# Kernel optimization log

Hardware: AMD Instinct MI355X
Metric: run time of the kernel (lower is better)

The kernel has to match this reference:

```python
import jax, jax.numpy as jnp
import numpy as np

RADIUS = 2  # matches LGA(radius=2)


def setup_inputs() -> dict:
    key = jax.random.key(0)
    k1, k2 = jax.random.split(key)
    N, C, H, W = 4, 32, 384, 768
    K = 2 * RADIUS + 1
    input1 = jax.random.normal(k1, (N, C, H, W), dtype=jnp.float32)
    input2 = jax.random.uniform(k2, (N, K * K, H, W), dtype=jnp.float32)
    return {"input1": input1, "input2": input2}


def reference(input1, input2):
    # Local Guided Aggregation (GANet LGA):
    # out[n,c,h,w] = sum_{i,j in (2r+1)^2} input1[n,c,h+i-r,w+j-r] * input2[n,i*K+j,h,w]
    # Per-pixel 5x5 filter shared across channels; zero padding at borders.
    r = RADIUS
    K = 2 * r + 1
    N, C, H, W = input1.shape
    padded = jnp.pad(input1, ((0, 0), (0, 0), (r, r), (r, r)))
    out = jnp.zeros_like(input1)
    for i in range(K):
        for j in range(K):
            # shifted window [N,C,H,W] times per-pixel tap weight [N,1,H,W]
            out = out + padded[:, :, i:i + H, j:j + W] * input2[:, i * K + j][:, None, :, :]
    return out
```

## Files before the change

### kernel.cpp

```cpp
#include <hip/hip_runtime.h>


#define N_DIM 4
#define C_DIM 32
#define H_DIM 384
#define W_DIM 768
#define HW (H_DIM * W_DIM)
#define TH 4
#define TW 256
#define LROWS (TH + 4)
#define LW 260
#define CHUNKS (LROWS * 65)

__global__ __launch_bounds__(256, 3)
void lga_kernel(const float* __restrict__ in1,
                const float* __restrict__ in2,
                float* __restrict__ out) {
    __shared__ float lds[2][LROWS * LW];

    const int tid = threadIdx.x;
    const int tx  = tid & 63;
    const int ty  = tid >> 6;
    const int w0  = blockIdx.x * TW;
    const int h0  = blockIdx.y * TH;
    const int n   = blockIdx.z;

    const int h  = h0 + ty;
    const int wb = w0 + 4 * tx;

    float4 wt[25];
    {
        const float* w_src = in2 + ((size_t)n * 25) * HW + (size_t)h * W_DIM + wb;
#pragma unroll
        for (int t = 0; t < 25; ++t) {
            float4 v = *(const float4*)(w_src + (size_t)t * HW);
            asm volatile("" : "+v"(v.x), "+v"(v.y), "+v"(v.z), "+v"(v.w));
            wt[t] = v;
        }
    }

    const float* in1_n = in1 + (size_t)n * C_DIM * HW;
    float*       out_n = out + (size_t)n * C_DIM * HW;

    int  soff[3];
    int  ldst[3];
    int  gcol[3];
    bool fast[3];
    bool rok[3];
    bool act[3];
#pragma unroll
    for (int k = 0; k < 3; ++k) {
        const int idx = tid + 256 * k;
        act[k] = (k < 2) || (tid < CHUNKS - 512);
        const int row = idx / 65;
        const int c4  = idx - row * 65;
        const int gh  = h0 - 2 + row;
        const int g   = w0 - 2 + 4 * c4;
        rok[k]  = (unsigned)gh < H_DIM;
        gcol[k] = g;
        fast[k] = rok[k] && (g >= 0) && (g + 3 < W_DIM);
        soff[k] = (rok[k] ? gh : 0) * W_DIM + g;
        ldst[k] = row * LW + 4 * c4;
    }

    auto load_chunk = [&](const float* src, int k) -> float4 {
        float4 v;
        if (fast[k]) {
            const float* p = src + soff[k];
            const float2 a = *(const float2*)p;
            const float2 b = *(const float2*)(p + 2);
            v = make_float4(a.x, a.y, b.x, b.y);
        } else {
            const int g = gcol[k];
            const float* prow = src + (soff[k] - g);
            v.x = (rok[k] && (unsigned)(g + 0) < W_DIM) ? prow[g + 0] : 0.f;
            v.y = (rok[k] && (unsigned)(g + 1) < W_DIM) ? prow[g + 1] : 0.f;
            v.z = (rok[k] && (unsigned)(g + 2) < W_DIM) ? prow[g + 2] : 0.f;
            v.w = (rok[k] && (unsigned)(g + 3) < W_DIM) ? prow[g + 3] : 0.f;
        }
        return v;
    };

    {
        float4 v0 = load_chunk(in1_n, 0);
        float4 v1 = load_chunk(in1_n, 1);
        float4 v2 = make_float4(0.f, 0.f, 0.f, 0.f);
        if (act[2]) v2 = load_chunk(in1_n, 2);
        *(float4*)&lds[0][ldst[0]] = v0;
        *(float4*)&lds[0][ldst[1]] = v1;
        if (act[2]) *(float4*)&lds[0][ldst[2]] = v2;
    }
    __syncthreads();

    for (int c = 0; c < C_DIM; ++c) {
        const int  cur  = c & 1;
        const bool more = (c + 1 < C_DIM);

        float4 n0, n1, n2 = make_float4(0.f, 0.f, 0.f, 0.f);
        if (more) {
            const float* src = in1_n + (size_t)(c + 1) * HW;
            n0 = load_chunk(src, 0);
            n1 = load_chunk(src, 1);
            if (act[2]) n2 = load_chunk(src, 2);
        }

        float acc0 = 0.f, acc1 = 0.f, acc2 = 0.f, acc3 = 0.f;
        const float* lbase = &lds[cur][0];
#pragma unroll
        for (int i = 0; i < 5; ++i) {
            const float* lrow = lbase + (ty + i) * LW + 4 * tx;
            const float4 A = *(const float4*)lrow;
            const float4 B = *(const float4*)(lrow + 4);
            const float win[8] = {A.x, A.y, A.z, A.w, B.x, B.y, B.z, B.w};
#pragma unroll
            for (int j = 0; j < 5; ++j) {
                const float4 wv = wt[5 * i + j];
                acc0 += wv.x * win[j + 0];
                acc1 += wv.y * win[j + 1];
                acc2 += wv.z * win[j + 2];
                acc3 += wv.w * win[j + 3];
            }
        }

        *(float4*)(out_n + (size_t)c * HW + (size_t)h * W_DIM + wb)
            = make_float4(acc0, acc1, acc2, acc3);

        if (more) {
            float* dst = &lds[cur ^ 1][0];
            *(float4*)&dst[ldst[0]] = n0;
            *(float4*)&dst[ldst[1]] = n1;
            if (act[2]) *(float4*)&dst[ldst[2]] = n2;
            __syncthreads();
        }
    }
}

extern "C" void kernel_launch(void* const* d_in, const int* in_sizes, int n_in,
                              void* d_out, int out_size, void* d_ws, size_t ws_size,
                              hipStream_t stream) {
    const float* in1 = (const float*)d_in[0];
    const float* in2 = (const float*)d_in[1];
    float* out = (float*)d_out;
    dim3 grid(W_DIM / TW, H_DIM / TH, N_DIM);
    lga_kernel<<<grid, 256, 0, stream>>>(in1, in2, out);
}
```

Baseline: 418.8 us.

## Split channels across blocks, reload weights per channel, remap block order

Splits the 32-channel loop across 4 workgroups per spatial tile, so the grid is 4x larger. The 25 per-pixel float4 weights are no longer held in registers; they are re-read from global memory (likely L1/L2 hits) inside every channel iteration, and the launch bound is raised to 6 blocks per SM. A 1D grid with a swizzled block index groups the channel-split blocks of one tile together for cache locality. The cost is four times more weight traffic and halo reloads against higher occupancy and parallelism.

```diff
diff --git a/kernel.cpp b/kernel.cpp
--- a/kernel.cpp
+++ b/kernel.cpp
@@ -8,39 +8,38 @@
 #define HW (H_DIM * W_DIM)
 #define TH 4
 #define TW 256
+#define CSPLIT 4
+#define CPB (C_DIM / CSPLIT)
 #define LROWS (TH + 4)
 #define LW 260
 #define CHUNKS (LROWS * 65)
+#define NTILE ((W_DIM / TW) * (H_DIM / TH) * N_DIM)
+#define NWG (NTILE * CSPLIT)
 
-__global__ __launch_bounds__(256, 3)
+__global__ __launch_bounds__(256, 6)
 void lga_kernel(const float* __restrict__ in1,
                 const float* __restrict__ in2,
                 float* __restrict__ out) {
     __shared__ float lds[2][LROWS * LW];
 
+    const int b = blockIdx.x;
+    const int T = (b & 7) * (NWG / 8) + (b >> 3);
+    const int cs = T & 3;
+    const int t  = T >> 2;
+    const int bx = t % 3;
+    const int by = (t / 3) % (H_DIM / TH);
+    const int n  = t / (3 * (H_DIM / TH));
+    const int c0 = cs * CPB;
+
     const int tid = threadIdx.x;
     const int tx  = tid & 63;
     const int ty  = tid >> 6;
-    const int w0  = blockIdx.x * TW;
-    const int h0  = blockIdx.y * TH;
-    const int n   = blockIdx.z;
+    const int w0  = bx * TW;
+    const int h0  = by * TH;
+    const int h   = h0 + ty;
+    const int wb  = w0 + 4 * tx;
 
-    const int h  = h0 + ty;
-    const int wb = w0 + 4 * tx;
-
-    float4 wt[25];
-    {
-        const float* w_src = in2 + ((size_t)n * 25) * HW + (size_t)h * W_DIM + wb;
-#pragma unroll
-        for (int t = 0; t < 25; ++t) {
-            float4 v = *(const float4*)(w_src + (size_t)t * HW);
-            asm volatile("" : "+v"(v.x), "+v"(v.y), "+v"(v.z), "+v"(v.w));
-            wt[t] = v;
-        }
-    }
-
-    const float* in1_n = in1 + (size_t)n * C_DIM * HW;
-    float*       out_n = out + (size_t)n * C_DIM * HW;
+    const float* w_src = in2 + ((size_t)n * 25) * HW + (size_t)h * W_DIM + wb;
 
     int  soff[3];
     int  ldst[3];
@@ -68,8 +67,8 @@
         if (fast[k]) {
             const float* p = src + soff[k];
             const float2 a = *(const float2*)p;
-            const float2 b = *(const float2*)(p + 2);
-            v = make_float4(a.x, a.y, b.x, b.y);
+            const float2 b2 = *(const float2*)(p + 2);
+            v = make_float4(a.x, a.y, b2.x, b2.y);
         } else {
             const int g = gcol[k];
             const float* prow = src + (soff[k] - g);
@@ -81,27 +80,31 @@
         return v;
     };
 
+    const float* src0 = in1 + (size_t)n * C_DIM * HW + (size_t)c0 * HW;
+    float*       dst  = out + (size_t)n * C_DIM * HW + (size_t)c0 * HW
+                            + (size_t)h * W_DIM + wb;
+
     {
-        float4 v0 = load_chunk(in1_n, 0);
-        float4 v1 = load_chunk(in1_n, 1);
+        float4 v0 = load_chunk(src0, 0);
+        float4 v1 = load_chunk(src0, 1);
         float4 v2 = make_float4(0.f, 0.f, 0.f, 0.f);
-        if (act[2]) v2 = load_chunk(in1_n, 2);
+        if (act[2]) v2 = load_chunk(src0, 2);
         *(float4*)&lds[0][ldst[0]] = v0;
         *(float4*)&lds[0][ldst[1]] = v1;
         if (act[2]) *(float4*)&lds[0][ldst[2]] = v2;
     }
     __syncthreads();
 
-    for (int c = 0; c < C_DIM; ++c) {
-        const int  cur  = c & 1;
-        const bool more = (c + 1 < C_DIM);
+    for (int cc = 0; cc < CPB; ++cc) {
+        const int  cur  = cc & 1;
+        const bool more = (cc + 1 < CPB);
 
         float4 n0, n1, n2 = make_float4(0.f, 0.f, 0.f, 0.f);
         if (more) {
-            const float* src = in1_n + (size_t)(c + 1) * HW;
-            n0 = load_chunk(src, 0);
-            n1 = load_chunk(src, 1);
-            if (act[2]) n2 = load_chunk(src, 2);
+            const float* srcn = src0 + (size_t)(cc + 1) * HW;
+            n0 = load_chunk(srcn, 0);
+            n1 = load_chunk(srcn, 1);
+            if (act[2]) n2 = load_chunk(srcn, 2);
         }
 
         float acc0 = 0.f, acc1 = 0.f, acc2 = 0.f, acc3 = 0.f;
@@ -112,24 +115,26 @@
             const float4 A = *(const float4*)lrow;
             const float4 B = *(const float4*)(lrow + 4);
             const float win[8] = {A.x, A.y, A.z, A.w, B.x, B.y, B.z, B.w};
+            float4 wv[5];
+#pragma unroll
+            for (int j = 0; j < 5; ++j)
+                wv[j] = *(const float4*)(w_src + (size_t)(5 * i + j) * HW);
 #pragma unroll
             for (int j = 0; j < 5; ++j) {
-                const float4 wv = wt[5 * i + j];
-                acc0 += wv.x * win[j + 0];
-                acc1 += wv.y * win[j + 1];
-                acc2 += wv.z * win[j + 2];
-                acc3 += wv.w * win[j + 3];
+                acc0 += wv[j].x * win[j + 0];
+                acc1 += wv[j].y * win[j + 1];
+                acc2 += wv[j].z * win[j + 2];
+                acc3 += wv[j].w * win[j + 3];
             }
         }
 
-        *(float4*)(out_n + (size_t)c * HW + (size_t)h * W_DIM + wb)
-            = make_float4(acc0, acc1, acc2, acc3);
+        *(float4*)(dst + (size_t)cc * HW) = make_float4(acc0, acc1, acc2, acc3);
 
         if (more) {
-            float* dst = &lds[cur ^ 1][0];
-            *(float4*)&dst[ldst[0]] = n0;
-            *(float4*)&dst[ldst[1]] = n1;
-            if (act[2]) *(float4*)&dst[ldst[2]] = n2;
+            float* dbuf = &lds[cur ^ 1][0];
+            *(float4*)&dbuf[ldst[0]] = n0;
+            *(float4*)&dbuf[ldst[1]] = n1;
+            if (act[2]) *(float4*)&dbuf[ldst[2]] = n2;
             __syncthreads();
         }
     }
@@ -141,6 +146,5 @@
     const float* in1 = (const float*)d_in[0];
     const float* in2 = (const float*)d_in[1];
     float* out = (float*)d_out;
-    dim3 grid(W_DIM / TW, H_DIM / TH, N_DIM);
-    lga_kernel<<<grid, 256, 0, stream>>>(in1, in2, out);
+    lga_kernel<<<dim3(NWG), 256, 0, stream>>>(in1, in2, out);
 }
```

Result: slower. 895.0 us (+113.7%).
